# Optimization experiments

Measured on AMD Instinct MI355X. Metric: run time of the kernel, lower is better.

Reference implementation:

```python
import jax, jax.numpy as jnp
import numpy as np

MASK_SCORE = -1.0e15
LOG_2PI = float(np.log(2.0 * np.pi))


def setup_inputs() -> dict:
    key = jax.random.key(0)
    k1, k2, k3, k4 = jax.random.split(key, 4)
    B, H, N, T = 32, 256, 512, 2048
    encoder_outputs = jax.random.normal(k1, (B, H, N), dtype=jnp.float32)
    # positive integer-like durations in [1, 7]
    durations = jnp.round(jax.random.uniform(k2, (B, N), minval=1.0, maxval=7.0)).astype(jnp.float32)
    # well-conditioned variances
    vars_ = jax.random.uniform(k3, (B, N), minval=0.5, maxval=2.0, dtype=jnp.float32)
    input_lengths = jax.random.randint(k4, (B,), N // 2, N + 1, dtype=jnp.int32)
    return {"encoder_outputs": encoder_outputs, "durations": durations,
            "vars": vars_, "input_lengths": input_lengths, "T": T}


def reference(encoder_outputs, durations, vars, input_lengths, T):
    # encoder_outputs: [B, H, N] -> [B, N, H]
    x = jnp.swapaxes(encoder_outputs, 1, 2)
    B, N, H = x.shape
    # Gaussian centers: cumsum(d) - d/2  -> [B, N]
    c = jnp.cumsum(durations, axis=1) - 0.5 * durations
    t = jnp.arange(T, dtype=x.dtype)  # [T]
    v = vars[:, :, None]              # [B, N, 1]
    # Gaussian log-density scores: [B, N, T]
    w_t = -0.5 * (LOG_2PI + jnp.log(v) + jnp.square(t[None, None, :] - c[:, :, None]) / v)
    # mask invalid phoneme positions (index >= length) along N
    invalid = jnp.arange(N)[None, :] >= input_lengths[:, None]  # [B, N]
    w_t = jnp.where(invalid[:, :, None], MASK_SCORE, w_t)
    # softmax over phoneme axis N, then weighted sum of encoder states
    w_t = jax.nn.softmax(w_t, axis=1)                 # [B, N, T]
    out = jnp.einsum('bnt,bnh->bth', w_t, x)          # [B, T, H]
    return jnp.swapaxes(out, 1, 2)                    # [B, H, T]
```

## Files before the change

### kernel.cpp

```cpp
#include <hip/hip_runtime.h>
#include <math.h>
#include <stdint.h>

static constexpr int B = 32, H = 256, N = 512, T = 2048;
static constexpr int TTILE = 64;
static constexpr int KC = 64;
static constexpr float kLOG_2PI = 1.8378770664093453f;
static constexpr float kLOG2E   = 1.4426950408889634f;
static constexpr float kNEG_BIG = -3.0e38f;
static constexpr float kRANGE_DELTA = 26.0f;

typedef __attribute__((ext_vector_type(8))) short bf16x8;
typedef __attribute__((ext_vector_type(4))) float f32x4;

static __device__ __forceinline__ short f2bf(float f) {
  unsigned u = __float_as_uint(f);
  unsigned r = (u + 0x7fffu + ((u >> 16) & 1u)) >> 16;
  return (short)r;
}

__global__ void k_prep(const float* __restrict__ dur, const float* __restrict__ vars,
                       const int* __restrict__ lens,
                       float4* __restrict__ psg, float2* __restrict__ bstat) {
  const int b = blockIdx.x;
  const int lane = threadIdx.x;
  const int L = lens[b];
  float running = 0.f;
  float rc[N / 64], ra2[N / 64], rq2[N / 64];
  float a2max = kNEG_BIG, a2min = -kNEG_BIG, q2min = -kNEG_BIG, q2max = kNEG_BIG;
  float dmax = 0.f, clast = 0.f;
#pragma unroll
  for (int i = 0; i < N / 64; ++i) {
    const int n = i * 64 + lane;
    const float d = dur[b * N + n];
    float x = d;
#pragma unroll
    for (int off = 1; off < 64; off <<= 1) {
      float up = __shfl_up(x, off, 64);
      if (lane >= off) x += up;
    }
    const float cc = running + x - 0.5f * d;
    running += __shfl(x, 63, 64);
    const float v = vars[b * N + n];
    const float a2v = -0.5f * (kLOG_2PI + logf(v)) * kLOG2E;
    const float q2v = 0.5f * kLOG2E / v;
    rc[i] = cc; ra2[i] = a2v; rq2[i] = q2v;
    if (n < L) {
      a2max = fmaxf(a2max, a2v); a2min = fminf(a2min, a2v);
      q2min = fminf(q2min, q2v); q2max = fmaxf(q2max, q2v);
      dmax = fmaxf(dmax, d);
      if (n == L - 1) clast = cc;
    }
  }
#pragma unroll
  for (int off = 32; off; off >>= 1) {
    a2max = fmaxf(a2max, __shfl_xor(a2max, off, 64));
    a2min = fminf(a2min, __shfl_xor(a2min, off, 64));
    q2min = fminf(q2min, __shfl_xor(q2min, off, 64));
    q2max = fmaxf(q2max, __shfl_xor(q2max, off, 64));
    dmax  = fmaxf(dmax,  __shfl_xor(dmax,  off, 64));
    clast = fmaxf(clast, __shfl_xor(clast, off, 64));
  }
  const float dnb = 0.5f * dmax;
  const float m_lower = a2min - q2max * dnb * dnb;
  const float thr = m_lower - kRANGE_DELTA;
#pragma unroll
  for (int i = 0; i < N / 64; ++i) {
    const int n = i * 64 + lane;
    const float rr = sqrtf(fmaxf(ra2[i] - thr, 0.f) / rq2[i]);
    psg[(size_t)b * N + n] = make_float4(rc[i], ra2[i], rq2[i], rr);
  }
  if (lane == 0) bstat[b] = make_float2(a2max, clast);
}

__global__ __launch_bounds__(256) void k_fused(
    const float* __restrict__ enc, const float4* __restrict__ psg,
    const int* __restrict__ lens, const float2* __restrict__ bstat,
    float* __restrict__ out) {
  __shared__ short pB[TTILE * KC];
  __shared__ float4 ps[N];
  __shared__ float m_lds[TTILE];
  __shared__ float s_lds[TTILE];
  __shared__ int range_sh[2];

  const int b = blockIdx.y;
  const int t0 = blockIdx.x * TTILE;
  const int tid = threadIdx.x;
  const int lane = tid & 63;
  const int wave = tid >> 6;
  const int L = lens[b];
  const float2 bs = bstat[b];
  const float* encb = enc + (size_t)b * H * N;
  const float4* psb = psg + (size_t)b * N;

  if (tid < TTILE) s_lds[tid] = 0.f;
  if (tid == 0) { range_sh[0] = N; range_sh[1] = -1; }
  __syncthreads();

  const bool tile_near = ((float)(t0 + TTILE - 1) <= bs.y);

  if (tile_near) {
    if (tid < TTILE) m_lds[tid] = bs.x;
    const float tmin = (float)t0, tmax = (float)(t0 + TTILE - 1);
    int lo = N, hi = -1;
#pragma unroll
    for (int rr = 0; rr < 2; ++rr) {
      const int n = rr * 256 + tid;
      const float4 p4 = psb[n];
      if (n < L && (p4.x - p4.w) <= tmax && (p4.x + p4.w) >= tmin) {
        lo = min(lo, n); hi = max(hi, n);
      }
    }
#pragma unroll
    for (int off = 32; off; off >>= 1) {
      lo = min(lo, __shfl_xor(lo, off, 64));
      hi = max(hi, __shfl_xor(hi, off, 64));
    }
    if (lane == 0) { atomicMin(&range_sh[0], lo); atomicMax(&range_sh[1], hi); }
    __syncthreads();
  } else {
    for (int i = tid; i < N; i += 256) ps[i] = psb[i];
    __syncthreads();
    const int tl = tid >> 2, j = tid & 3;
    const float tf = (float)(t0 + tl);
    const int iL = (L + 3) >> 2;
    float mA = kNEG_BIG, mB = kNEG_BIG;
    int i1 = 0;
    for (; i1 + 1 < iL; i1 += 2) {
      const int n1 = i1 * 4 + j, n2 = n1 + 4;
      const float4 p1 = ps[n1];
      const float tc1 = tf - p1.x;
      const float w1 = fmaf(-p1.z, tc1 * tc1, p1.y);
      mA = fmaxf(mA, (n1 < L) ? w1 : kNEG_BIG);
      const float4 p2 = ps[n2];
      const float tc2 = tf - p2.x;
      const float w2 = fmaf(-p2.z, tc2 * tc2, p2.y);
      mB = fmaxf(mB, (n2 < L) ? w2 : kNEG_BIG);
    }
    if (i1 < iL) {
      const int n1 = i1 * 4 + j;
      const float4 p1 = ps[n1];
      const float tc1 = tf - p1.x;
      const float w1 = fmaf(-p1.z, tc1 * tc1, p1.y);
      mA = fmaxf(mA, (n1 < L) ? w1 : kNEG_BIG);
    }
    float m = fmaxf(mA, mB);
    m = fmaxf(m, __shfl_xor(m, 1, 64));
    m = fmaxf(m, __shfl_xor(m, 2, 64));
    if (j == 0) m_lds[tl] = m;

    const float thr = m - kRANGE_DELTA;
    int lo = N, hi = -1;
    for (int i2 = 0; i2 < iL; ++i2) {
      const int n = i2 * 4 + j;
      const float4 p4 = ps[n];
      const float tc = tf - p4.x;
      const float ww = fmaf(-p4.z, tc * tc, p4.y);
      if (n < L && ww >= thr) { lo = min(lo, n); hi = max(hi, n); }
    }
#pragma unroll
    for (int off = 32; off; off >>= 1) {
      lo = min(lo, __shfl_xor(lo, off, 64));
      hi = max(hi, __shfl_xor(hi, off, 64));
    }
    if (lane == 0) { atomicMin(&range_sh[0], lo); atomicMax(&range_sh[1], hi); }
    __syncthreads();
  }

  int nlo = range_sh[0], nhi = range_sh[1];
  if (nhi < 0) { nlo = 0; nhi = L - 1; }
  nlo = max(0, min(nlo, N - 1)); nhi = max(nlo, min(nhi, N - 1));

  f32x4 acc[4][4];
#pragma unroll
  for (int mf = 0; mf < 4; ++mf)
#pragma unroll
    for (int tt = 0; tt < 4; ++tt) acc[mf][tt] = (f32x4){0.f, 0.f, 0.f, 0.f};

  const int l15 = lane & 15;
  const int lhi = lane >> 4;
  const int arow0 = wave * 64 + l15;

  int wb = nlo & ~3;
  while (true) {
    const int wbc = min(wb, N - KC);
    const int wlo = max(wb, nlo);
    __syncthreads();
#pragma unroll
    for (int i = 0; i < 2; ++i) {
      const int flat = i * 256 + tid;
      const int t = flat >> 3, j8 = flat & 7;
      const int nbase = wbc + j8 * 8;
      const int byte = ((t * KC + j8 * 8) * 2) ^ ((t & 7) << 4);
      bf16x8 w;
      float psum = 0.f;
      if (nbase + 7 < wlo || nbase > nhi) {
        w = (bf16x8){0, 0, 0, 0, 0, 0, 0, 0};
      } else {
        const float mt = m_lds[t];
        const float tft = (float)(t0 + t);
#pragma unroll
        for (int jj = 0; jj < 8; ++jj) {
          const int n = nbase + jj;
          const float4 p4 = psb[min(n, nhi)];
          const float tc = tft - p4.x;
          const float w2v = fmaf(-p4.z, tc * tc, p4.y);
          const float pv = (n >= wlo && n <= nhi) ? exp2f(w2v - mt) : 0.f;
          psum += pv;
          w[jj] = f2bf(pv);
        }
      }
      *(bf16x8*)((char*)pB + byte) = w;
      psum += __shfl_xor(psum, 1, 64);
      psum += __shfl_xor(psum, 2, 64);
      psum += __shfl_xor(psum, 4, 64);
      if ((tid & 7) == 0) atomicAdd(&s_lds[t], psum);
    }
    __syncthreads();
#pragma unroll
    for (int kk = 0; kk < KC; kk += 32) {
      if (wbc + kk > nhi || wbc + kk + 31 < wlo) continue;
      const int col = wbc + kk + lhi * 8;
      bf16x8 aF[4], bF[4];
#pragma unroll
      for (int mf = 0; mf < 4; ++mf) {
        const float* src = encb + (size_t)(arow0 + mf * 16) * N + col;
        const float4 v0 = *(const float4*)(src);
        const float4 v1 = *(const float4*)(src + 4);
        aF[mf][0] = f2bf(v0.x); aF[mf][1] = f2bf(v0.y);
        aF[mf][2] = f2bf(v0.z); aF[mf][3] = f2bf(v0.w);
        aF[mf][4] = f2bf(v1.x); aF[mf][5] = f2bf(v1.y);
        aF[mf][6] = f2bf(v1.z); aF[mf][7] = f2bf(v1.w);
      }
#pragma unroll
      for (int tt = 0; tt < 4; ++tt) {
        const int t = tt * 16 + l15;
        const int byte = ((t * KC + kk + lhi * 8) * 2) ^ ((t & 7) << 4);
        bF[tt] = *(const bf16x8*)((const char*)pB + byte);
      }
#pragma unroll
      for (int mf = 0; mf < 4; ++mf)
#pragma unroll
        for (int tt = 0; tt < 4; ++tt)
          acc[mf][tt] = __builtin_amdgcn_mfma_f32_16x16x32_bf16(aF[mf], bF[tt], acc[mf][tt], 0, 0, 0);
    }
    if (wbc + KC > nhi) break;
    wb = wbc + KC;
  }

#pragma unroll
  for (int tt = 0; tt < 4; ++tt) {
    const int t = tt * 16 + l15;
    const float is = 1.0f / s_lds[t];
#pragma unroll
    for (int mf = 0; mf < 4; ++mf) {
      const int h = wave * 64 + mf * 16 + lhi * 4;
#pragma unroll
      for (int r = 0; r < 4; ++r) {
        out[((size_t)(b * H + h + r)) * T + t0 + t] = acc[mf][tt][r] * is;
      }
    }
  }
}

extern "C" void kernel_launch(void* const* d_in, const int* in_sizes, int n_in,
                              void* d_out, int out_size, void* d_ws, size_t ws_size,
                              hipStream_t stream) {
  const float* enc  = (const float*)d_in[0];
  const float* dur  = (const float*)d_in[1];
  const float* vars = (const float*)d_in[2];
  const int*   lens = (const int*)d_in[3];
  float* out = (float*)d_out;

  char* ws = (char*)d_ws;
  float4* psg   = (float4*)ws;
  float2* bstat = (float2*)(psg + B * N);

  k_prep<<<B, 64, 0, stream>>>(dur, vars, lens, psg, bstat);
  k_fused<<<dim3(T / TTILE, B), 256, 0, stream>>>(enc, psg, lens, bstat, out);
}
```

Measured before the change: 40.34 us.

## Compute softmax weights in registers per wave, removing LDS staging and barriers

Each wave now computes the exp weights for its own MFMA B-fragment directly in registers instead of staging them cooperatively in LDS. The LDS weight tile, the shared row-sum atomics and the per-chunk __syncthreads are removed, and the normalising sums are reduced with cross-lane shuffles at the end. In the near-tile path each wave also finds the phoneme range on its own, with no block barrier. The cost is redundant work: all four waves recompute the same weight matrix and each reloads the per-phoneme parameters from global memory, in exchange for fewer synchronisation stalls and less LDS traffic.

```diff
diff --git a/kernel.cpp b/kernel.cpp
--- a/kernel.cpp
+++ b/kernel.cpp
@@ -77,10 +77,8 @@
     const float* __restrict__ enc, const float4* __restrict__ psg,
     const int* __restrict__ lens, const float2* __restrict__ bstat,
     float* __restrict__ out) {
-  __shared__ short pB[TTILE * KC];
   __shared__ float4 ps[N];
   __shared__ float m_lds[TTILE];
-  __shared__ float s_lds[TTILE];
   __shared__ int range_sh[2];
 
   const int b = blockIdx.y;
@@ -93,19 +91,20 @@
   const float* encb = enc + (size_t)b * H * N;
   const float4* psb = psg + (size_t)b * N;
 
-  if (tid < TTILE) s_lds[tid] = 0.f;
-  if (tid == 0) { range_sh[0] = N; range_sh[1] = -1; }
-  __syncthreads();
+  const int l15 = lane & 15;
+  const int lhi = lane >> 4;
+  const int arow0 = wave * 64 + l15;
 
   const bool tile_near = ((float)(t0 + TTILE - 1) <= bs.y);
+  int nlo, nhi;
+  float mt[4];
 
   if (tile_near) {
-    if (tid < TTILE) m_lds[tid] = bs.x;
     const float tmin = (float)t0, tmax = (float)(t0 + TTILE - 1);
     int lo = N, hi = -1;
 #pragma unroll
-    for (int rr = 0; rr < 2; ++rr) {
-      const int n = rr * 256 + tid;
+    for (int rr = 0; rr < 8; ++rr) {
+      const int n = rr * 64 + lane;
       const float4 p4 = psb[n];
       if (n < L && (p4.x - p4.w) <= tmax && (p4.x + p4.w) >= tmin) {
         lo = min(lo, n); hi = max(hi, n);
@@ -116,9 +115,11 @@
       lo = min(lo, __shfl_xor(lo, off, 64));
       hi = max(hi, __shfl_xor(hi, off, 64));
     }
-    if (lane == 0) { atomicMin(&range_sh[0], lo); atomicMax(&range_sh[1], hi); }
-    __syncthreads();
+    nlo = lo; nhi = hi;
+#pragma unroll
+    for (int tt = 0; tt < 4; ++tt) mt[tt] = bs.x;
   } else {
+    if (tid == 0) { range_sh[0] = N; range_sh[1] = -1; }
     for (int i = tid; i < N; i += 256) ps[i] = psb[i];
     __syncthreads();
     const int tl = tid >> 2, j = tid & 3;
@@ -165,9 +166,11 @@
     }
     if (lane == 0) { atomicMin(&range_sh[0], lo); atomicMax(&range_sh[1], hi); }
     __syncthreads();
-  }
-
-  int nlo = range_sh[0], nhi = range_sh[1];
+    nlo = range_sh[0]; nhi = range_sh[1];
+#pragma unroll
+    for (int tt = 0; tt < 4; ++tt) mt[tt] = m_lds[tt * 16 + l15];
+  }
+
   if (nhi < 0) { nlo = 0; nhi = L - 1; }
   nlo = max(0, min(nlo, N - 1)); nhi = max(nlo, min(nhi, N - 1));
 
@@ -176,52 +179,21 @@
   for (int mf = 0; mf < 4; ++mf)
 #pragma unroll
     for (int tt = 0; tt < 4; ++tt) acc[mf][tt] = (f32x4){0.f, 0.f, 0.f, 0.f};
-
-  const int l15 = lane & 15;
-  const int lhi = lane >> 4;
-  const int arow0 = wave * 64 + l15;
+  float psum[4] = {0.f, 0.f, 0.f, 0.f};
 
   int wb = nlo & ~3;
   while (true) {
     const int wbc = min(wb, N - KC);
     const int wlo = max(wb, nlo);
-    __syncthreads();
-#pragma unroll
-    for (int i = 0; i < 2; ++i) {
-      const int flat = i * 256 + tid;
-      const int t = flat >> 3, j8 = flat & 7;
-      const int nbase = wbc + j8 * 8;
-      const int byte = ((t * KC + j8 * 8) * 2) ^ ((t & 7) << 4);
-      bf16x8 w;
-      float psum = 0.f;
-      if (nbase + 7 < wlo || nbase > nhi) {
-        w = (bf16x8){0, 0, 0, 0, 0, 0, 0, 0};
-      } else {
-        const float mt = m_lds[t];
-        const float tft = (float)(t0 + t);
-#pragma unroll
-        for (int jj = 0; jj < 8; ++jj) {
-          const int n = nbase + jj;
-          const float4 p4 = psb[min(n, nhi)];
-          const float tc = tft - p4.x;
-          const float w2v = fmaf(-p4.z, tc * tc, p4.y);
-          const float pv = (n >= wlo && n <= nhi) ? exp2f(w2v - mt) : 0.f;
-          psum += pv;
-          w[jj] = f2bf(pv);
-        }
-      }
-      *(bf16x8*)((char*)pB + byte) = w;
-      psum += __shfl_xor(psum, 1, 64);
-      psum += __shfl_xor(psum, 2, 64);
-      psum += __shfl_xor(psum, 4, 64);
-      if ((tid & 7) == 0) atomicAdd(&s_lds[t], psum);
-    }
-    __syncthreads();
 #pragma unroll
     for (int kk = 0; kk < KC; kk += 32) {
-      if (wbc + kk > nhi || wbc + kk + 31 < wlo) continue;
-      const int col = wbc + kk + lhi * 8;
-      bf16x8 aF[4], bF[4];
+      const int colk = wbc + kk;
+      if (colk > nhi || colk + 31 < wlo) continue;
+      const int col = colk + lhi * 8;
+      float4 pq[8];
+#pragma unroll
+      for (int jj = 0; jj < 8; ++jj) pq[jj] = psb[col + jj];
+      bf16x8 aF[4];
 #pragma unroll
       for (int mf = 0; mf < 4; ++mf) {
         const float* src = encb + (size_t)(arow0 + mf * 16) * N + col;
@@ -234,15 +206,24 @@
       }
 #pragma unroll
       for (int tt = 0; tt < 4; ++tt) {
-        const int t = tt * 16 + l15;
-        const int byte = ((t * KC + kk + lhi * 8) * 2) ^ ((t & 7) << 4);
-        bF[tt] = *(const bf16x8*)((const char*)pB + byte);
-      }
-#pragma unroll
-      for (int mf = 0; mf < 4; ++mf)
-#pragma unroll
-        for (int tt = 0; tt < 4; ++tt)
-          acc[mf][tt] = __builtin_amdgcn_mfma_f32_16x16x32_bf16(aF[mf], bF[tt], acc[mf][tt], 0, 0, 0);
+        const float tft = (float)(t0 + tt * 16 + l15);
+        const float mtt = mt[tt];
+        bf16x8 bF;
+        float psv = 0.f;
+#pragma unroll
+        for (int jj = 0; jj < 8; ++jj) {
+          const int n = col + jj;
+          const float tc = tft - pq[jj].x;
+          const float w2v = fmaf(-pq[jj].z, tc * tc, pq[jj].y);
+          const float pv = (n >= wlo && n <= nhi) ? exp2f(w2v - mtt) : 0.f;
+          psv += pv;
+          bF[jj] = f2bf(pv);
+        }
+        psum[tt] += psv;
+#pragma unroll
+        for (int mf = 0; mf < 4; ++mf)
+          acc[mf][tt] = __builtin_amdgcn_mfma_f32_16x16x32_bf16(aF[mf], bF, acc[mf][tt], 0, 0, 0);
+      }
     }
     if (wbc + KC > nhi) break;
     wb = wbc + KC;
@@ -250,8 +231,11 @@
 
 #pragma unroll
   for (int tt = 0; tt < 4; ++tt) {
+    float s = psum[tt];
+    s += __shfl_xor(s, 16, 64);
+    s += __shfl_xor(s, 32, 64);
+    const float is = 1.0f / s;
     const int t = tt * 16 + l15;
-    const float is = 1.0f / s_lds[t];
 #pragma unroll
     for (int mf = 0; mf < 4; ++mf) {
       const int h = wave * 64 + mf * 16 + lhi * 4;
```

Result: slower. 41.38 us (+2.6%).
